# Kernel tuning notes

Measured on AMD Instinct MI355X. Metric: run time of the kernel, lower is better.

Reference implementation:

```python
import jax, jax.numpy as jnp
import numpy as np

B, H, T, DK = 4, 8, 2048, 64

def setup_inputs() -> dict:
    key = jax.random.key(0)
    kq, kk, kv, kb = jax.random.split(key, 4)
    return {
        "Q": jax.random.normal(kq, (B, H, T, DK), dtype=jnp.float32),
        "K": jax.random.normal(kk, (B, H, T, DK), dtype=jnp.float32),
        "V": jax.random.normal(kv, (B, H, T, DK), dtype=jnp.float32),
        "attn_bias": jax.random.normal(kb, (H, T, T), dtype=jnp.float32),
    }

def reference(Q, K, V, attn_bias):
    # scores = Q K^T / sqrt(d_k) + bias  (bias added post-scaling, as in source)
    d_k = Q.shape[-1]
    scale = 1.0 / jnp.sqrt(jnp.asarray(d_k, Q.dtype))
    scores = jnp.einsum("bhqd,bhkd->bhqk", Q, K) * scale + attn_bias
    attn_weights = jax.nn.softmax(scores, axis=-1)  # (B,H,T,T), rows sum to 1
    # Dropout is identity in eval/reference mode; output uses (pre-dropout) weights.
    output = jnp.einsum("bhqk,bhkd->bhqd", attn_weights, V)
    return (output, attn_weights)
```

## Files before the change

### kernel.cpp

```cpp
#include <hip/hip_runtime.h>
#include <hip/hip_bf16.h>

#define TT   2048
#define DKK  64
#define NHH  8
#define NBB  4
#define QB   128
#define KBLK 64
#define NKT  (TT / KBLK)
#define LDE  72
#define TILE (KBLK * LDE)
#define SCALE 0.125f

#define SOFT_BARRIER() do {                                         \
    asm volatile("s_waitcnt lgkmcnt(0)" ::: "memory");              \
    __builtin_amdgcn_s_barrier();                                   \
    asm volatile("" ::: "memory");                                  \
} while (0)

typedef __attribute__((ext_vector_type(4))) float  f32x4;
typedef __attribute__((ext_vector_type(8))) __bf16 bf16x8;
typedef __attribute__((ext_vector_type(4))) __bf16 bf16x4;

__global__ __launch_bounds__(256)
void cast_k_kernel(const float* __restrict__ K, __bf16* __restrict__ Kb) {
    size_t i = ((size_t)blockIdx.x * 256 + threadIdx.x) * 8;
    f32x4 a = *(const f32x4*)(K + i);
    f32x4 b = *(const f32x4*)(K + i + 4);
    bf16x8 o = {(__bf16)a[0], (__bf16)a[1], (__bf16)a[2], (__bf16)a[3],
                (__bf16)b[0], (__bf16)b[1], (__bf16)b[2], (__bf16)b[3]};
    *(bf16x8*)(Kb + i) = o;
}

__global__ __launch_bounds__(256)
void vt_kernel(const float* __restrict__ V, __bf16* __restrict__ Vt) {
    __shared__ __bf16 tile[DKK][72];
    const int bh = blockIdx.y;
    const int t0 = blockIdx.x * 64;
    const int tid = threadIdx.x;
    const float* Vb = V + ((size_t)bh * TT + t0) * DKK;
    #pragma unroll
    for (int i = 0; i < 4; ++i) {
        int idx = tid + i * 256;
        int row = idx >> 4, c4 = idx & 15;
        f32x4 v = *(const f32x4*)(Vb + row * DKK + c4 * 4);
        tile[c4 * 4 + 0][row] = (__bf16)v[0];
        tile[c4 * 4 + 1][row] = (__bf16)v[1];
        tile[c4 * 4 + 2][row] = (__bf16)v[2];
        tile[c4 * 4 + 3][row] = (__bf16)v[3];
    }
    __syncthreads();
    __bf16* out = Vt + (size_t)bh * DKK * TT + t0;
    #pragma unroll
    for (int i = 0; i < 2; ++i) {
        int idx = tid + i * 256;
        int d = idx >> 3, ch = idx & 7;
        bf16x8 o = *(const bf16x8*)&tile[d][ch * 8];
        *(bf16x8*)(out + (size_t)d * TT + ch * 8) = o;
    }
}

__global__ __launch_bounds__(512, 4)
void sdpa_main(const float* __restrict__ Qp, const float* __restrict__ Bp,
               const __bf16* __restrict__ Kb, const __bf16* __restrict__ Vt,
               float* __restrict__ Op, float* __restrict__ Wp)
{
    __shared__ __bf16 Kl[2][TILE];
    __shared__ __bf16 Vl[2][TILE];
    __shared__ __bf16 Pl[8][16 * LDE];

    const int tid  = threadIdx.x;
    const int lane = tid & 63;
    const int w    = tid >> 6;
    const int g    = lane >> 4;
    const int ql   = lane & 15;

    const int id  = blockIdx.x;
    const int h   = id & 7;
    const int r   = id >> 3;
    const int qt  = r & 15;
    const int b   = r >> 4;
    const int bh  = b * NHH + h;

    const int q_local = w * 16 + ql;
    const int q_glob  = qt * QB + q_local;

    const __bf16* Kbh = Kb + (size_t)bh * TT * DKK;
    const __bf16* Vbh = Vt + (size_t)bh * DKK * TT;
    const float* biasRow = Bp + ((size_t)h * TT + q_glob) * TT;

    const int srow = tid >> 3;
    const int sch  = tid & 7;

    const float* qrow = Qp + ((size_t)bh * TT + q_glob) * DKK;
    f32x4 qa = *(const f32x4*)(qrow + g * 8);
    f32x4 qc = *(const f32x4*)(qrow + g * 8 + 4);
    f32x4 qe = *(const f32x4*)(qrow + 32 + g * 8);
    f32x4 qf = *(const f32x4*)(qrow + 32 + g * 8 + 4);
    const bf16x8 qfrag0 = {(__bf16)qa[0], (__bf16)qa[1], (__bf16)qa[2], (__bf16)qa[3],
                           (__bf16)qc[0], (__bf16)qc[1], (__bf16)qc[2], (__bf16)qc[3]};
    const bf16x8 qfrag1 = {(__bf16)qe[0], (__bf16)qe[1], (__bf16)qe[2], (__bf16)qe[3],
                           (__bf16)qf[0], (__bf16)qf[1], (__bf16)qf[2], (__bf16)qf[3]};

    *(bf16x8*)&Kl[0][srow * LDE + sch * 8] =
        *(const bf16x8*)(Kbh + (size_t)srow * DKK + sch * 8);
    __syncthreads();

    f32x4 lacc = {0.f, 0.f, 0.f, 0.f};
    for (int kt = 0; kt < NKT; ++kt) {
        const int cur = kt & 1;
        const bool more = (kt + 1 < NKT);
        bf16x8 kreg;
        if (more)
            kreg = *(const bf16x8*)(Kbh + ((size_t)(kt + 1) * KBLK + srow) * DKK + sch * 8);
        const float* bp = biasRow + kt * KBLK;
        f32x4 bv[4];
        #pragma unroll
        for (int s = 0; s < 4; ++s) bv[s] = *(const f32x4*)(bp + s * 16 + g * 4);

        f32x4 acc[4] = {};
        #pragma unroll
        for (int s = 0; s < 4; ++s) {
            bf16x8 a0 = *(const bf16x8*)&Kl[cur][(s * 16 + ql) * LDE + g * 8];
            acc[s] = __builtin_amdgcn_mfma_f32_16x16x32_bf16(a0, qfrag0, acc[s], 0, 0, 0);
            bf16x8 a1 = *(const bf16x8*)&Kl[cur][(s * 16 + ql) * LDE + 32 + g * 8];
            acc[s] = __builtin_amdgcn_mfma_f32_16x16x32_bf16(a1, qfrag1, acc[s], 0, 0, 0);
        }
        #pragma unroll
        for (int s = 0; s < 4; ++s) {
            f32x4 x = acc[s] * SCALE + bv[s];
            lacc[0] += __expf(x[0]);
            lacc[1] += __expf(x[1]);
            lacc[2] += __expf(x[2]);
            lacc[3] += __expf(x[3]);
        }
        if (more)
            *(bf16x8*)&Kl[cur ^ 1][srow * LDE + sch * 8] = kreg;
        SOFT_BARRIER();
    }
    float l_run = lacc[0] + lacc[1] + lacc[2] + lacc[3];
    l_run += __shfl_xor(l_run, 16);
    l_run += __shfl_xor(l_run, 32);
    const float inv_l = 1.0f / l_run;

    *(bf16x8*)&Kl[0][srow * LDE + sch * 8] =
        *(const bf16x8*)(Kbh + (size_t)srow * DKK + sch * 8);
    *(bf16x8*)&Vl[0][srow * LDE + sch * 8] =
        *(const bf16x8*)(Vbh + (size_t)srow * TT + sch * 8);
    __syncthreads();

    f32x4 oacc[4] = {};
    for (int kt = 0; kt < NKT; ++kt) {
        const int cur = kt & 1;
        const bool more = (kt + 1 < NKT);
        bf16x8 kreg, vreg;
        if (more) {
            kreg = *(const bf16x8*)(Kbh + ((size_t)(kt + 1) * KBLK + srow) * DKK + sch * 8);
            vreg = *(const bf16x8*)(Vbh + (size_t)srow * TT + (kt + 1) * KBLK + sch * 8);
        }
        const float* bp = biasRow + kt * KBLK;
        f32x4 bv[4];
        #pragma unroll
        for (int s = 0; s < 4; ++s) bv[s] = *(const f32x4*)(bp + s * 16 + g * 4);

        f32x4 acc[4] = {};
        #pragma unroll
        for (int s = 0; s < 4; ++s) {
            bf16x8 a0 = *(const bf16x8*)&Kl[cur][(s * 16 + ql) * LDE + g * 8];
            acc[s] = __builtin_amdgcn_mfma_f32_16x16x32_bf16(a0, qfrag0, acc[s], 0, 0, 0);
            bf16x8 a1 = *(const bf16x8*)&Kl[cur][(s * 16 + ql) * LDE + 32 + g * 8];
            acc[s] = __builtin_amdgcn_mfma_f32_16x16x32_bf16(a1, qfrag1, acc[s], 0, 0, 0);
        }
        #pragma unroll
        for (int s = 0; s < 4; ++s) {
            f32x4 x = acc[s] * SCALE + bv[s];
            bf16x4 pb = {(__bf16)(__expf(x[0]) * inv_l), (__bf16)(__expf(x[1]) * inv_l),
                         (__bf16)(__expf(x[2]) * inv_l), (__bf16)(__expf(x[3]) * inv_l)};
            *(bf16x4*)&Pl[w][ql * LDE + s * 16 + g * 4] = pb;
        }
        const bf16x8 bp0 = *(const bf16x8*)&Pl[w][ql * LDE + g * 8];
        const bf16x8 bp1 = *(const bf16x8*)&Pl[w][ql * LDE + 32 + g * 8];
        #pragma unroll
        for (int m = 0; m < 4; ++m) {
            bf16x8 av0 = *(const bf16x8*)&Vl[cur][(m * 16 + ql) * LDE + g * 8];
            oacc[m] = __builtin_amdgcn_mfma_f32_16x16x32_bf16(av0, bp0, oacc[m], 0, 0, 0);
            bf16x8 av1 = *(const bf16x8*)&Vl[cur][(m * 16 + ql) * LDE + 32 + g * 8];
            oacc[m] = __builtin_amdgcn_mfma_f32_16x16x32_bf16(av1, bp1, oacc[m], 0, 0, 0);
        }
        #pragma unroll
        for (int s2 = 0; s2 < 4; ++s2) {
            const int wr = s2 * 4 + g;
            bf16x4 pw = *(const bf16x4*)&Pl[w][wr * LDE + ql * 4];
            f32x4 ow = {(float)pw[0], (float)pw[1], (float)pw[2], (float)pw[3]};
            __builtin_nontemporal_store(ow,
                (f32x4*)(Wp + ((size_t)bh * TT + qt * QB + w * 16 + wr) * TT
                             + kt * KBLK + ql * 4));
        }
        if (more) {
            *(bf16x8*)&Kl[cur ^ 1][srow * LDE + sch * 8] = kreg;
            *(bf16x8*)&Vl[cur ^ 1][srow * LDE + sch * 8] = vreg;
        }
        SOFT_BARRIER();
    }

    float* Orow = Op + ((size_t)bh * TT + q_glob) * DKK;
    #pragma unroll
    for (int m = 0; m < 4; ++m)
        __builtin_nontemporal_store(oacc[m], (f32x4*)(Orow + m * 16 + g * 4));
}

extern "C" void kernel_launch(void* const* d_in, const int* in_sizes, int n_in,
                              void* d_out, int out_size, void* d_ws, size_t ws_size,
                              hipStream_t stream) {
    const float* Q  = (const float*)d_in[0];
    const float* K  = (const float*)d_in[1];
    const float* V  = (const float*)d_in[2];
    const float* Bs = (const float*)d_in[3];
    float* Out = (float*)d_out;
    float* W   = Out + (size_t)NBB * NHH * TT * DKK;

    const size_t nElem = (size_t)NBB * NHH * TT * DKK;
    __bf16* Kb = (__bf16*)d_ws;
    __bf16* Vt = Kb + nElem;

    cast_k_kernel<<<dim3(nElem / 8 / 256), dim3(256), 0, stream>>>(K, Kb);
    vt_kernel<<<dim3(TT / 64, NBB * NHH), dim3(256), 0, stream>>>(V, Vt);
    sdpa_main<<<dim3((TT / QB) * NBB * NHH), dim3(512), 0, stream>>>(Q, Bs, Kb, Vt, Out, W);
}
```

Before: 204.9 us.

## Split softmax row-sum pass into separate kernel with finer grid and split-K waves

New measurement: 222.4 us. 8.5% more time.

```diff
diff --git a/kernel.cpp b/kernel.cpp
--- a/kernel.cpp
+++ b/kernel.cpp
@@ -5,7 +5,6 @@
 #define DKK  64
 #define NHH  8
 #define NBB  4
-#define QB   128
 #define KBLK 64
 #define NKT  (TT / KBLK)
 #define LDE  72
@@ -60,33 +59,32 @@
     }
 }
 
-__global__ __launch_bounds__(512, 4)
-void sdpa_main(const float* __restrict__ Qp, const float* __restrict__ Bp,
-               const __bf16* __restrict__ Kb, const __bf16* __restrict__ Vt,
-               float* __restrict__ Op, float* __restrict__ Wp)
+__global__ __launch_bounds__(512, 8)
+void lsum_kernel(const float* __restrict__ Qp, const float* __restrict__ Bp,
+                 const __bf16* __restrict__ Kb, float* __restrict__ Lp)
 {
     __shared__ __bf16 Kl[2][TILE];
-    __shared__ __bf16 Vl[2][TILE];
-    __shared__ __bf16 Pl[8][16 * LDE];
+    __shared__ float  Sst[8][16];
 
     const int tid  = threadIdx.x;
     const int lane = tid & 63;
     const int w    = tid >> 6;
+    const int kg   = w >> 2;
+    const int qw   = w & 3;
     const int g    = lane >> 4;
     const int ql   = lane & 15;
 
     const int id  = blockIdx.x;
     const int h   = id & 7;
     const int r   = id >> 3;
-    const int qt  = r & 15;
-    const int b   = r >> 4;
+    const int qt  = r & 31;
+    const int b   = r >> 5;
     const int bh  = b * NHH + h;
 
-    const int q_local = w * 16 + ql;
-    const int q_glob  = qt * QB + q_local;
+    const int q_local = qw * 16 + ql;
+    const int q_glob  = qt * 64 + q_local;
 
     const __bf16* Kbh = Kb + (size_t)bh * TT * DKK;
-    const __bf16* Vbh = Vt + (size_t)bh * DKK * TT;
     const float* biasRow = Bp + ((size_t)h * TT + q_glob) * TT;
 
     const int srow = tid >> 3;
@@ -113,21 +111,22 @@
         bf16x8 kreg;
         if (more)
             kreg = *(const bf16x8*)(Kbh + ((size_t)(kt + 1) * KBLK + srow) * DKK + sch * 8);
-        const float* bp = biasRow + kt * KBLK;
-        f32x4 bv[4];
-        #pragma unroll
-        for (int s = 0; s < 4; ++s) bv[s] = *(const f32x4*)(bp + s * 16 + g * 4);
-
-        f32x4 acc[4] = {};
-        #pragma unroll
-        for (int s = 0; s < 4; ++s) {
-            bf16x8 a0 = *(const bf16x8*)&Kl[cur][(s * 16 + ql) * LDE + g * 8];
+        const float* bp = biasRow + kt * KBLK + kg * 32;
+        f32x4 bv[2];
+        #pragma unroll
+        for (int s = 0; s < 2; ++s) bv[s] = *(const f32x4*)(bp + s * 16 + g * 4);
+
+        f32x4 acc[2] = {};
+        #pragma unroll
+        for (int s = 0; s < 2; ++s) {
+            const int krow = (kg * 2 + s) * 16 + ql;
+            bf16x8 a0 = *(const bf16x8*)&Kl[cur][krow * LDE + g * 8];
             acc[s] = __builtin_amdgcn_mfma_f32_16x16x32_bf16(a0, qfrag0, acc[s], 0, 0, 0);
-            bf16x8 a1 = *(const bf16x8*)&Kl[cur][(s * 16 + ql) * LDE + 32 + g * 8];
+            bf16x8 a1 = *(const bf16x8*)&Kl[cur][krow * LDE + 32 + g * 8];
             acc[s] = __builtin_amdgcn_mfma_f32_16x16x32_bf16(a1, qfrag1, acc[s], 0, 0, 0);
         }
         #pragma unroll
-        for (int s = 0; s < 4; ++s) {
+        for (int s = 0; s < 2; ++s) {
             f32x4 x = acc[s] * SCALE + bv[s];
             lacc[0] += __expf(x[0]);
             lacc[1] += __expf(x[1]);
@@ -141,7 +140,57 @@
     float l_run = lacc[0] + lacc[1] + lacc[2] + lacc[3];
     l_run += __shfl_xor(l_run, 16);
     l_run += __shfl_xor(l_run, 32);
-    const float inv_l = 1.0f / l_run;
+    if (g == 0) Sst[w][ql] = l_run;
+    __syncthreads();
+    l_run += Sst[w ^ 4][ql];
+    if (kg == 0 && g == 0)
+        Lp[(size_t)bh * TT + q_glob] = l_run;
+}
+
+__global__ __launch_bounds__(512, 4)
+void sdpa_main(const float* __restrict__ Qp, const float* __restrict__ Bp,
+               const __bf16* __restrict__ Kb, const __bf16* __restrict__ Vt,
+               const float* __restrict__ Lp,
+               float* __restrict__ Op, float* __restrict__ Wp)
+{
+    __shared__ __bf16 Kl[2][TILE];
+    __shared__ __bf16 Vl[2][TILE];
+    __shared__ __bf16 Pl[8][16 * LDE];
+
+    const int tid  = threadIdx.x;
+    const int lane = tid & 63;
+    const int w    = tid >> 6;
+    const int g    = lane >> 4;
+    const int ql   = lane & 15;
+
+    const int id  = blockIdx.x;
+    const int h   = id & 7;
+    const int r   = id >> 3;
+    const int qt  = r & 15;
+    const int b   = r >> 4;
+    const int bh  = b * NHH + h;
+
+    const int q_local = w * 16 + ql;
+    const int q_glob  = qt * 128 + q_local;
+
+    const __bf16* Kbh = Kb + (size_t)bh * TT * DKK;
+    const __bf16* Vbh = Vt + (size_t)bh * DKK * TT;
+    const float* biasRow = Bp + ((size_t)h * TT + q_glob) * TT;
+
+    const int srow = tid >> 3;
+    const int sch  = tid & 7;
+
+    const float* qrow = Qp + ((size_t)bh * TT + q_glob) * DKK;
+    f32x4 qa = *(const f32x4*)(qrow + g * 8);
+    f32x4 qc = *(const f32x4*)(qrow + g * 8 + 4);
+    f32x4 qe = *(const f32x4*)(qrow + 32 + g * 8);
+    f32x4 qf = *(const f32x4*)(qrow + 32 + g * 8 + 4);
+    const bf16x8 qfrag0 = {(__bf16)qa[0], (__bf16)qa[1], (__bf16)qa[2], (__bf16)qa[3],
+                           (__bf16)qc[0], (__bf16)qc[1], (__bf16)qc[2], (__bf16)qc[3]};
+    const bf16x8 qfrag1 = {(__bf16)qe[0], (__bf16)qe[1], (__bf16)qe[2], (__bf16)qe[3],
+                           (__bf16)qf[0], (__bf16)qf[1], (__bf16)qf[2], (__bf16)qf[3]};
+
+    const float inv_l = 1.0f / Lp[(size_t)bh * TT + q_glob];
 
     *(bf16x8*)&Kl[0][srow * LDE + sch * 8] =
         *(const bf16x8*)(Kbh + (size_t)srow * DKK + sch * 8);
@@ -193,7 +242,7 @@
             bf16x4 pw = *(const bf16x4*)&Pl[w][wr * LDE + ql * 4];
             f32x4 ow = {(float)pw[0], (float)pw[1], (float)pw[2], (float)pw[3]};
             __builtin_nontemporal_store(ow,
-                (f32x4*)(Wp + ((size_t)bh * TT + qt * QB + w * 16 + wr) * TT
+                (f32x4*)(Wp + ((size_t)bh * TT + qt * 128 + w * 16 + wr) * TT
                              + kt * KBLK + ql * 4));
         }
         if (more) {
@@ -222,8 +271,10 @@
     const size_t nElem = (size_t)NBB * NHH * TT * DKK;
     __bf16* Kb = (__bf16*)d_ws;
     __bf16* Vt = Kb + nElem;
+    float*  Lp = (float*)(Vt + nElem);
 
     cast_k_kernel<<<dim3(nElem / 8 / 256), dim3(256), 0, stream>>>(K, Kb);
     vt_kernel<<<dim3(TT / 64, NBB * NHH), dim3(256), 0, stream>>>(V, Vt);
-    sdpa_main<<<dim3((TT / QB) * NBB * NHH), dim3(512), 0, stream>>>(Q, Bs, Kb, Vt, Out, W);
-}
+    lsum_kernel<<<dim3(32 * NBB * NHH), dim3(512), 0, stream>>>(Q, Bs, Kb, Lp);
+    sdpa_main<<<dim3(16 * NBB * NHH), dim3(512), 0, stream>>>(Q, Bs, Kb, Vt, Lp, Out, W);
+}
```
